# Optimization experiments

Measured on AMD Instinct MI355X. Metric: run time of the kernel, lower is better.

Reference implementation:

```python
import jax, jax.numpy as jnp
import numpy as np

B, C, H, W = 16, 512, 32, 32
CI = C // 2
EPS = 1e-5


def _lin_params(k, din, dout):
    kw, kb = jax.random.split(k)
    w = jax.random.normal(kw, (dout, din), jnp.float32) * (1.0 / np.sqrt(din))
    b = jax.random.normal(kb, (dout,), jnp.float32) * 0.01
    return w, b


def _bn_params(k):
    k1, k2, k3, k4 = jax.random.split(k, 4)
    g = 1.0 + 0.05 * jax.random.normal(k1, (C,), jnp.float32)
    b = 0.05 * jax.random.normal(k2, (C,), jnp.float32)
    m = 0.1 * jax.random.normal(k3, (C,), jnp.float32)
    v = jax.random.uniform(k4, (C,), jnp.float32, 0.5, 1.5)
    return g, b, m, v


def setup_inputs() -> dict:
    key = jax.random.key(0)
    ks = jax.random.split(key, 12)
    inp = {
        'rgb_cm': jax.random.normal(ks[0], (B, C, H, W), jnp.float32),
        'flow_cm': jax.random.normal(ks[1], (B, C, H, W), jnp.float32),
    }
    for i, pfx in enumerate(['1', '2']):
        g, b, m, v = _bn_params(ks[2 + 5 * i])
        inp[f'bn{pfx}_g'], inp[f'bn{pfx}_b'] = g, b
        inp[f'bn{pfx}_m'], inp[f'bn{pfx}_v'] = m, v
        inp[f'th{pfx}_w'], inp[f'th{pfx}_b'] = _lin_params(ks[3 + 5 * i], C, CI)
        inp[f'ph{pfx}_w'], inp[f'ph{pfx}_b'] = _lin_params(ks[4 + 5 * i], C, CI)
        inp[f'g{pfx}_w'], inp[f'g{pfx}_b'] = _lin_params(ks[5 + 5 * i], C, CI)
        inp[f'w{pfx}_w'], inp[f'w{pfx}_b'] = _lin_params(ks[6 + 5 * i], CI, C)
    return inp


def _bn_relu(x, g, b, m, v):
    # x: [B, C, num]; eval-mode BatchNorm1d over channel dim, then ReLU
    scale = (g * jax.lax.rsqrt(v + EPS))[None, :, None]
    shift = (b - m * g * jax.lax.rsqrt(v + EPS))[None, :, None]
    return jax.nn.relu(x * scale + shift)


def _can(A, Bx, bn_g, bn_b, bn_m, bn_v, th_w, th_b, ph_w, ph_b, g_w, g_b, w_w, w_b):
    # A, Bx: [B, C, num]
    A = _bn_relu(A, bn_g, bn_b, bn_m, bn_v).transpose(0, 2, 1)   # [B, num, C]
    Bx = _bn_relu(Bx, bn_g, bn_b, bn_m, bn_v).transpose(0, 2, 1)  # [B, num, C]
    x_theta = A @ th_w.T + th_b      # [B, num, CI]
    x_phi = Bx @ ph_w.T + ph_b       # [B, num, CI]
    attn = jnp.einsum('bnc,bmc->bnm', x_theta, x_phi)  # [B, num, num] (unscaled)
    f_div_C = jax.nn.softmax(attn, axis=-1)
    g_x = A @ g_w.T + g_b            # [B, num, CI]
    y = jnp.einsum('bnm,bmc->bnc', f_div_C, g_x)
    W_y = y @ w_w.T + w_b            # [B, num, C]
    return (A + W_y).transpose(0, 2, 1)  # [B, C, num]


def reference(rgb_cm, flow_cm,
              bn1_g, bn1_b, bn1_m, bn1_v, th1_w, th1_b, ph1_w, ph1_b, g1_w, g1_b, w1_w, w1_b,
              bn2_g, bn2_b, bn2_m, bn2_v, th2_w, th2_b, ph2_w, ph2_b, g2_w, g2_b, w2_w, w2_b):
    b, c, h, w = rgb_cm.shape
    rgb_f = rgb_cm.reshape(b, c, h * w)
    flow_f = flow_cm.reshape(b, c, h * w)
    att_rgb = _can(rgb_f, flow_f, bn1_g, bn1_b, bn1_m, bn1_v,
                   th1_w, th1_b, ph1_w, ph1_b, g1_w, g1_b, w1_w, w1_b)
    att_flow = _can(flow_f, rgb_f, bn2_g, bn2_b, bn2_m, bn2_v,
                    th2_w, th2_b, ph2_w, ph2_b, g2_w, g2_b, w2_w, w2_b)
    return att_rgb.reshape(b, c, h, w), att_flow.reshape(b, c, h, w)
```

## Files before the change

kernel.cpp:

```cpp
#include <hip/hip_runtime.h>


typedef __bf16 bf16x8 __attribute__((ext_vector_type(8)));
typedef float  f32x4  __attribute__((ext_vector_type(4)));
typedef float  f32x16 __attribute__((ext_vector_type(16)));
typedef unsigned u32x4 __attribute__((ext_vector_type(4)));
static_assert(sizeof(bf16x8) == 16, "bf16x8 must be 16B");

constexpr int KTILE = 8704;
constexpr int VTILE = 10240;
constexpr int KINST = 32 * KTILE;
constexpr int VINST = 32 * VTILE;

__device__ __forceinline__ ushort f2bf(float x) {
  unsigned u = __builtin_bit_cast(unsigned, x);
  u = (u + 0x7fffu + ((u >> 16) & 1u)) >> 16;
  return (ushort)u;
}
__device__ __forceinline__ unsigned packbf(float lo, float hi) {
  return (unsigned)f2bf(lo) | ((unsigned)f2bf(hi) << 16);
}
__device__ __forceinline__ void gload_lds16(const ushort* g, ushort* l) {
  __builtin_amdgcn_global_load_lds(
      (const __attribute__((address_space(1))) void*)g,
      (__attribute__((address_space(3))) void*)l, 16, 0, 0);
}

struct WcvtArgs { const float* src[8]; };
__global__ __launch_bounds__(256) void wcvt8_k(WcvtArgs a, ushort* __restrict__ dst) {
  const int which = blockIdx.y;
  const int i = (blockIdx.x * 256 + threadIdx.x) * 4;
  float4 x = *reinterpret_cast<const float4*>(a.src[which] + i);
  ushort4 u = {f2bf(x.x), f2bf(x.y), f2bf(x.z), f2bf(x.w)};
  *reinterpret_cast<ushort4*>(dst + (size_t)which * 131072 + i) = u;
}

__global__ __launch_bounds__(256) void bn2_k(
    const float* __restrict__ rgb, const float* __restrict__ flow,
    const float* __restrict__ g1, const float* __restrict__ b1,
    const float* __restrict__ m1, const float* __restrict__ v1,
    const float* __restrict__ g2, const float* __restrict__ b2,
    const float* __restrict__ m2, const float* __restrict__ v2,
    ushort* __restrict__ Abn1, ushort* __restrict__ Bbn1,
    ushort* __restrict__ Abn2, ushort* __restrict__ Bbn2)
{
  const int z = blockIdx.z;
  const int b = z >> 1, which = z & 1;
  const float* src = which ? flow : rgb;
  ushort* o1 = which ? Bbn1 : Abn1;
  ushort* o2 = which ? Abn2 : Bbn2;
  src += (size_t)b * 512 * 1024;
  o1  += (size_t)b * 1024 * 512;
  o2  += (size_t)b * 1024 * 512;

  __shared__ unsigned tileU[32][36];
  const int n0 = blockIdx.x * 32, c0 = blockIdx.y * 32;

  const int rc = threadIdx.x >> 3, nq = threadIdx.x & 7;
  {
    const int c = c0 + rc;
    const float s1 = g1[c] * rsqrtf(v1[c] + 1e-5f);
    const float h1 = b1[c] - m1[c] * s1;
    const float s2 = g2[c] * rsqrtf(v2[c] + 1e-5f);
    const float h2 = b2[c] - m2[c] * s2;
    float4 x = *reinterpret_cast<const float4*>(src + (size_t)c * 1024 + n0 + nq * 4);
    u32x4 u;
    u[0] = packbf(fmaxf(x.x * s1 + h1, 0.f), fmaxf(x.x * s2 + h2, 0.f));
    u[1] = packbf(fmaxf(x.y * s1 + h1, 0.f), fmaxf(x.y * s2 + h2, 0.f));
    u[2] = packbf(fmaxf(x.z * s1 + h1, 0.f), fmaxf(x.z * s2 + h2, 0.f));
    u[3] = packbf(fmaxf(x.w * s1 + h1, 0.f), fmaxf(x.w * s2 + h2, 0.f));
    *reinterpret_cast<u32x4*>(&tileU[rc][nq * 4]) = u;
  }
  __syncthreads();
  const int r = threadIdx.x >> 3, cq = threadIdx.x & 7;
  ushort4 w1, w2;
  {
    const unsigned u0 = tileU[cq * 4 + 0][r];
    const unsigned u1 = tileU[cq * 4 + 1][r];
    const unsigned u2 = tileU[cq * 4 + 2][r];
    const unsigned u3 = tileU[cq * 4 + 3][r];
    w1 = (ushort4){(ushort)(u0 & 0xffff), (ushort)(u1 & 0xffff),
                   (ushort)(u2 & 0xffff), (ushort)(u3 & 0xffff)};
    w2 = (ushort4){(ushort)(u0 >> 16), (ushort)(u1 >> 16),
                   (ushort)(u2 >> 16), (ushort)(u3 >> 16)};
  }
  const size_t base = (size_t)(n0 + r) * 512 + c0 + cq * 4;
  *reinterpret_cast<ushort4*>(o1 + base) = w1;
  *reinterpret_cast<ushort4*>(o2 + base) = w2;
}

struct ProjDesc { const ushort* W; const ushort* act; const float* bias;
                  ushort* out; int mode; };
struct ProjArgs { ProjDesc d[6]; };

__global__ __launch_bounds__(256, 2) void proj128_k(ProjArgs pa) {
  __shared__ __align__(16) ushort Al[128 * 80];
  __shared__ __align__(16) ushort Bl[128 * 80];

  const int bx = blockIdx.x;
  const int mb = bx >> 3, nb = bx & 7;
  const int by = blockIdx.y;
  const ProjDesc d = pa.d[by >> 4];
  const int inst = by & 15;
  const ushort* A = d.W;
  const ushort* Bact = d.act + (size_t)inst * 524288;

  const int tid = threadIdx.x;
  const int w = tid >> 6, lane = tid & 63;
  const int q = lane >> 4, lm = lane & 15;
  const int m0 = mb * 128, n0 = nb * 128;

  int row[4], c8[4];
  #pragma unroll
  for (int i = 0; i < 4; ++i) { int g = i * 256 + tid; row[i] = g >> 3; c8[i] = g & 7; }

  bf16x8 ast[4], bst[4];
  auto sload = [&](int kk) {
    #pragma unroll
    for (int i = 0; i < 4; ++i) {
      ast[i] = *reinterpret_cast<const bf16x8*>(A + (size_t)(m0 + row[i]) * 512 + kk + c8[i] * 8);
      bst[i] = *reinterpret_cast<const bf16x8*>(Bact + (size_t)(n0 + row[i]) * 512 + kk + c8[i] * 8);
    }
  };
  sload(0);

  f32x4 acc[4][4];
  #pragma unroll
  for (int i = 0; i < 4; ++i)
    #pragma unroll
    for (int j = 0; j < 4; ++j) acc[i][j] = (f32x4){0.f, 0.f, 0.f, 0.f};

  const int wm = (w >> 1) * 64, wn = (w & 1) * 64;

  for (int t = 0; t < 8; ++t) {
    __syncthreads();
    #pragma unroll
    for (int i = 0; i < 4; ++i) {
      *reinterpret_cast<bf16x8*>(Al + row[i] * 80 + c8[i] * 8) = ast[i];
      *reinterpret_cast<bf16x8*>(Bl + row[i] * 80 + c8[i] * 8) = bst[i];
    }
    __syncthreads();
    if (t < 7) sload((t + 1) * 64);
    #pragma unroll
    for (int ks = 0; ks < 2; ++ks) {
      bf16x8 af[4], bfr[4];
      #pragma unroll
      for (int f = 0; f < 4; ++f)
        af[f] = *reinterpret_cast<const bf16x8*>(Al + (wm + f * 16 + lm) * 80 + ks * 32 + q * 8);
      #pragma unroll
      for (int f = 0; f < 4; ++f)
        bfr[f] = *reinterpret_cast<const bf16x8*>(Bl + (wn + f * 16 + lm) * 80 + ks * 32 + q * 8);
      __builtin_amdgcn_s_setprio(1);
      #pragma unroll
      for (int fi = 0; fi < 4; ++fi)
        #pragma unroll
        for (int fj = 0; fj < 4; ++fj)
          acc[fi][fj] = __builtin_amdgcn_mfma_f32_16x16x32_bf16(af[fi], bfr[fj], acc[fi][fj], 0, 0, 0);
      __builtin_amdgcn_s_setprio(0);
    }
  }

  if (d.mode == 0) {
    ushort* out = d.out + (size_t)inst * 262144;
    #pragma unroll
    for (int fi = 0; fi < 4; ++fi)
      #pragma unroll
      for (int fj = 0; fj < 4; ++fj) {
        const int m4 = m0 + wm + fi * 16 + q * 4;
        const int n  = n0 + wn + fj * 16 + lm;
        float4 bi = *reinterpret_cast<const float4*>(d.bias + m4);
        ushort4 u = {f2bf(acc[fi][fj][0] + bi.x), f2bf(acc[fi][fj][1] + bi.y),
                     f2bf(acc[fi][fj][2] + bi.z), f2bf(acc[fi][fj][3] + bi.w)};
        *reinterpret_cast<ushort4*>(out + (size_t)n * 256 + m4) = u;
      }
  } else if (d.mode == 1) {
    ushort* out = d.out + (size_t)inst * KINST;
    #pragma unroll
    for (int fi = 0; fi < 4; ++fi)
      #pragma unroll
      for (int fj = 0; fj < 4; ++fj) {
        const int m4 = m0 + wm + fi * 16 + q * 4;
        const int n  = n0 + wn + fj * 16 + lm;
        float4 bi = *reinterpret_cast<const float4*>(d.bias + m4);
        ushort4 u = {f2bf(acc[fi][fj][0] + bi.x), f2bf(acc[fi][fj][1] + bi.y),
                     f2bf(acc[fi][fj][2] + bi.z), f2bf(acc[fi][fj][3] + bi.w)};
        *reinterpret_cast<ushort4*>(out + (size_t)(n >> 5) * KTILE + (n & 31) * 264 + m4) = u;
      }
  } else {
    ushort* out = d.out + (size_t)inst * VINST;
    #pragma unroll
    for (int fi = 0; fi < 4; ++fi)
      #pragma unroll
      for (int fj = 0; fj < 4; ++fj) {
        const int n = n0 + wn + fj * 16 + lm;
        const size_t base = (size_t)(n >> 5) * VTILE + ((n & 31) >> 3) * 8 + (n & 7);
        #pragma unroll
        for (int j = 0; j < 4; ++j) {
          const int m = m0 + wm + fi * 16 + q * 4 + j;
          out[base + (size_t)m * 40] = f2bf(acc[fi][fj][j] + d.bias[m]);
        }
      }
  }
}

__global__ __launch_bounds__(256, 2) void flash_k(
    const ushort* __restrict__ Qp, const ushort* __restrict__ Kg,
    const ushort* __restrict__ Vg, ushort* __restrict__ Op)
{
  __shared__ __align__(16) ushort KV[2][KTILE + VTILE];
  __shared__ float2 stat2[2][32];

  const int raw = blockIdx.x;
  const int xcd = raw & 7, loc = raw >> 3;
  const int inst = xcd * 4 + (loc >> 4);
  const int qb = loc & 15;

  const int tid = threadIdx.x;
  const int w = tid >> 6, lane = tid & 63;
  const int u = w & 1, p = w >> 1;
  const int h = lane >> 5, lm5 = lane & 31;

  const ushort* Q  = Qp + (size_t)inst * 262144;
  const ushort* Kt = Kg + (size_t)inst * KINST + (size_t)p * 16 * KTILE;
  const ushort* Vt = Vg + (size_t)inst * VINST + (size_t)p * 16 * VTILE;

  ushort* Klds = &KV[p][0];
  ushort* Vlds = &KV[p][KTILE];

  const int nrow0 = qb * 64 + u * 32;

  bf16x8 qf[16];
  #pragma unroll
  for (int cs = 0; cs < 16; ++cs)
    qf[cs] = *reinterpret_cast<const bf16x8*>(
        Q + (size_t)(nrow0 + lm5) * 256 + cs * 16 + h * 8);

  f32x16 acc[8];
  #pragma unroll
  for (int cb = 0; cb < 8; ++cb)
    #pragma unroll
    for (int i = 0; i < 16; ++i) acc[cb][i] = 0.f;

  float run_m = -__builtin_inff();
  float run_l = 0.f;

  auto stageK = [&](int t) {
    const ushort* src = Kt + (size_t)t * KTILE;
    const int base = u ? 9 : 0;
    #pragma unroll
    for (int j = 0; j < 9; ++j)
      if (u == 0 || j < 8)
        gload_lds16(src + (base + j) * 512 + lane * 8, Klds + (base + j) * 512);
  };
  auto stageV = [&](int t) {
    const ushort* src = Vt + (size_t)t * VTILE;
    #pragma unroll
    for (int j = 0; j < 10; ++j)
      gload_lds16(src + (u * 10 + j) * 512 + lane * 8, Vlds + (u * 10 + j) * 512);
  };

  stageK(0);
  stageV(0);
  asm volatile("s_waitcnt vmcnt(0)" ::: "memory");
  __builtin_amdgcn_sched_barrier(0);
  __builtin_amdgcn_s_barrier();

  for (int t = 0; t < 16; ++t) {
    f32x16 S;
    #pragma unroll
    for (int i = 0; i < 16; ++i) S[i] = 0.f;
    __builtin_amdgcn_s_setprio(1);
    #pragma unroll
    for (int cs = 0; cs < 16; ++cs) {
      bf16x8 kf = *reinterpret_cast<const bf16x8*>(
          Klds + lm5 * 264 + (cs * 2 + h) * 8);
      S = __builtin_amdgcn_mfma_f32_32x32x16_bf16(kf, qf[cs], S, 0, 0, 0);
    }
    __builtin_amdgcn_s_setprio(0);

    __builtin_amdgcn_sched_barrier(0);
    asm volatile("s_waitcnt vmcnt(0)" ::: "memory");
    __builtin_amdgcn_sched_barrier(0);
    __builtin_amdgcn_s_barrier();
    __builtin_amdgcn_sched_barrier(0);
    if (t < 15) stageK(t + 1);

    float ml = fmaxf(fmaxf(fmaxf(S[0], S[1]), fmaxf(S[2], S[3])),
                     fmaxf(fmaxf(S[4], S[5]), fmaxf(S[6], S[7])));
    ml = fmaxf(ml, fmaxf(fmaxf(fmaxf(S[8], S[9]), fmaxf(S[10], S[11])),
                         fmaxf(fmaxf(S[12], S[13]), fmaxf(S[14], S[15]))));
    ml = fmaxf(ml, __shfl_xor(ml, 32));
    const float mnew = fmaxf(run_m, ml);
    if (!__all(ml <= run_m + 8.f)) {
      const float sc = __expf(run_m - mnew);
      run_m = mnew;
      run_l *= sc;
      #pragma unroll
      for (int cb = 0; cb < 8; ++cb) acc[cb] *= sc;
    }
    #pragma unroll
    for (int i = 0; i < 16; ++i) S[i] = __expf(S[i] - run_m);
    float ts = ((S[0] + S[1]) + (S[2] + S[3])) + ((S[4] + S[5]) + (S[6] + S[7]));
    ts += ((S[8] + S[9]) + (S[10] + S[11])) + ((S[12] + S[13]) + (S[14] + S[15]));
    ts += __shfl_xor(ts, 32);
    run_l += ts;

    const unsigned pk0 = packbf(S[0], S[1]),   pk1 = packbf(S[2], S[3]);
    const unsigned pk2 = packbf(S[4], S[5]),   pk3 = packbf(S[6], S[7]);
    const unsigned pk4 = packbf(S[8], S[9]),   pk5 = packbf(S[10], S[11]);
    const unsigned pk6 = packbf(S[12], S[13]), pk7 = packbf(S[14], S[15]);
    const unsigned sx0 = __shfl_xor(pk0, 32), sx1 = __shfl_xor(pk1, 32);
    const unsigned sx2 = __shfl_xor(pk2, 32), sx3 = __shfl_xor(pk3, 32);
    const unsigned sx4 = __shfl_xor(pk4, 32), sx5 = __shfl_xor(pk5, 32);
    const unsigned sx6 = __shfl_xor(pk6, 32), sx7 = __shfl_xor(pk7, 32);
    const bool hh = (h != 0);
    u32x4 B0, B1;
    B0[0] = hh ? sx2 : pk0;  B0[1] = hh ? sx3 : pk1;
    B0[2] = hh ? pk2 : sx0;  B0[3] = hh ? pk3 : sx1;
    B1[0] = hh ? sx6 : pk4;  B1[1] = hh ? sx7 : pk5;
    B1[2] = hh ? pk6 : sx4;  B1[3] = hh ? pk7 : sx5;
    const bf16x8 pf0 = __builtin_bit_cast(bf16x8, B0);
    const bf16x8 pf1 = __builtin_bit_cast(bf16x8, B1);

    __builtin_amdgcn_s_setprio(1);
    #pragma unroll
    for (int cb = 0; cb < 8; ++cb) {
      bf16x8 v0 = *reinterpret_cast<const bf16x8*>(
          Vlds + (cb * 32 + lm5) * 40 + h * 8);
      bf16x8 v1 = *reinterpret_cast<const bf16x8*>(
          Vlds + (cb * 32 + lm5) * 40 + (2 + h) * 8);
      acc[cb] = __builtin_amdgcn_mfma_f32_32x32x16_bf16(v0, pf0, acc[cb], 0, 0, 0);
      acc[cb] = __builtin_amdgcn_mfma_f32_32x32x16_bf16(v1, pf1, acc[cb], 0, 0, 0);
    }
    __builtin_amdgcn_s_setprio(0);

    __builtin_amdgcn_sched_barrier(0);
    __builtin_amdgcn_s_barrier();
    __builtin_amdgcn_sched_barrier(0);
    if (t < 15) {
      stageV(t + 1);
      asm volatile("s_waitcnt vmcnt(10)" ::: "memory");
    } else {
      asm volatile("s_waitcnt vmcnt(0)" ::: "memory");
    }
    __builtin_amdgcn_sched_barrier(0);
    __builtin_amdgcn_s_barrier();
    __builtin_amdgcn_sched_barrier(0);
  }

  __syncthreads();
  if (p == 1 && lane < 32) stat2[u][lm5] = make_float2(run_m, run_l);

  float a0 = 1.f, a1 = 0.f, inv = 1.f;
  float4* mb = reinterpret_cast<float4*>(&KV[0][0]);
  #pragma unroll
  for (int half = 0; half < 2; ++half) {
    __syncthreads();
    if (p == 1) {
      #pragma unroll
      for (int cb2 = 0; cb2 < 4; ++cb2) {
        const int cb = half * 4 + cb2;
        #pragma unroll
        for (int r4 = 0; r4 < 4; ++r4) {
          float4 v = {acc[cb][r4 * 4 + 0], acc[cb][r4 * 4 + 1],
                      acc[cb][r4 * 4 + 2], acc[cb][r4 * 4 + 3]};
          mb[u * 1024 + cb2 * 256 + r4 * 64 + lane] = v;
        }
      }
    }
    __syncthreads();
    if (p == 0) {
      if (half == 0) {
        const float2 s1 = stat2[u][lm5];
        const float M = fmaxf(run_m, s1.x);
        a0 = __expf(run_m - M);
        a1 = __expf(s1.x - M);
        inv = 1.f / (a0 * run_l + a1 * s1.y);
      }
      ushort* Ob = Op + (size_t)inst * 262144 + (size_t)(nrow0 + lm5) * 256;
      #pragma unroll
      for (int cb2 = 0; cb2 < 4; ++cb2) {
        const int cb = half * 4 + cb2;
        #pragma unroll
        for (int r4 = 0; r4 < 4; ++r4) {
          float4 o = mb[u * 1024 + cb2 * 256 + r4 * 64 + lane];
          ushort4 s;
          s.x = f2bf((a0 * acc[cb][r4 * 4 + 0] + a1 * o.x) * inv);
          s.y = f2bf((a0 * acc[cb][r4 * 4 + 1] + a1 * o.y) * inv);
          s.z = f2bf((a0 * acc[cb][r4 * 4 + 2] + a1 * o.z) * inv);
          s.w = f2bf((a0 * acc[cb][r4 * 4 + 3] + a1 * o.w) * inv);
          *reinterpret_cast<ushort4*>(Ob + cb * 32 + r4 * 8 + h * 4) = s;
        }
      }
    }
  }
}

struct WgemmArgs {
  const ushort* yb[2]; const ushort* wW[2]; const float* wb[2];
  const float* src[2]; const float* g[2]; const float* bb[2];
  const float* mm[2]; const float* vv[2];
};

__global__ __launch_bounds__(256, 2) void wgemm_epi_k(WgemmArgs a, float* __restrict__ outp) {
  __shared__ __align__(16) ushort Al[128 * 80];
  __shared__ __align__(16) ushort Bl[128 * 80];

  const int bx = blockIdx.x;
  const int mb = bx >> 2, nb = bx & 3;
  const int by = blockIdx.y;
  const int mod = by >> 4, b = by & 15;

  const ushort* A  = a.yb[mod] + (size_t)b * 262144;
  const ushort* Bw = a.wW[mod];
  const float* wb  = a.wb[mod];
  const float* src = a.src[mod] + (size_t)b * 512 * 1024;
  const float* g   = a.g[mod];
  const float* bbp = a.bb[mod];
  const float* mm  = a.mm[mod];
  const float* vv  = a.vv[mod];
  float* out = outp + (size_t)mod * 16 * 512 * 1024 + (size_t)b * 512 * 1024;

  const int tid = threadIdx.x;
  const int w = tid >> 6, lane = tid & 63;
  const int q = lane >> 4, lm = lane & 15;
  const int m0 = mb * 128, n0 = nb * 128;

  int row[4], c8[4];
  #pragma unroll
  for (int i = 0; i < 4; ++i) { int gg = i * 256 + tid; row[i] = gg >> 3; c8[i] = gg & 7; }

  bf16x8 ast[4], bst[4];
  auto sload = [&](int kk) {
    #pragma unroll
    for (int i = 0; i < 4; ++i) {
      ast[i] = *reinterpret_cast<const bf16x8*>(A  + (size_t)(m0 + row[i]) * 256 + kk + c8[i] * 8);
      bst[i] = *reinterpret_cast<const bf16x8*>(Bw + (size_t)(n0 + row[i]) * 256 + kk + c8[i] * 8);
    }
  };
  sload(0);

  f32x4 acc[4][4];
  #pragma unroll
  for (int i = 0; i < 4; ++i)
    #pragma unroll
    for (int j = 0; j < 4; ++j) acc[i][j] = (f32x4){0.f, 0.f, 0.f, 0.f};

  const int wm = (w >> 1) * 64, wn = (w & 1) * 64;

  for (int t = 0; t < 4; ++t) {
    __syncthreads();
    #pragma unroll
    for (int i = 0; i < 4; ++i) {
      *reinterpret_cast<bf16x8*>(Al + row[i] * 80 + c8[i] * 8) = ast[i];
      *reinterpret_cast<bf16x8*>(Bl + row[i] * 80 + c8[i] * 8) = bst[i];
    }
    __syncthreads();
    if (t < 3) sload((t + 1) * 64);
    #pragma unroll
    for (int ks = 0; ks < 2; ++ks) {
      bf16x8 af[4], bfr[4];
      #pragma unroll
      for (int f = 0; f < 4; ++f)
        af[f] = *reinterpret_cast<const bf16x8*>(Al + (wm + f * 16 + lm) * 80 + ks * 32 + q * 8);
      #pragma unroll
      for (int f = 0; f < 4; ++f)
        bfr[f] = *reinterpret_cast<const bf16x8*>(Bl + (wn + f * 16 + lm) * 80 + ks * 32 + q * 8);
      __builtin_amdgcn_s_setprio(1);
      #pragma unroll
      for (int fi = 0; fi < 4; ++fi)
        #pragma unroll
        for (int fj = 0; fj < 4; ++fj)
          acc[fi][fj] = __builtin_amdgcn_mfma_f32_16x16x32_bf16(af[fi], bfr[fj], acc[fi][fj], 0, 0, 0);
      __builtin_amdgcn_s_setprio(0);
    }
  }

  #pragma unroll
  for (int fj = 0; fj < 4; ++fj) {
    const int c = n0 + wn + fj * 16 + lm;
    const float sc = g[c] * rsqrtf(vv[c] + 1e-5f);
    const float sh = bbp[c] - mm[c] * sc;
    const float bv = wb[c];
    #pragma unroll
    for (int fi = 0; fi < 4; ++fi) {
      const int n4 = m0 + wm + fi * 16 + q * 4;
      const size_t base = (size_t)c * 1024 + n4;
      float4 x = *reinterpret_cast<const float4*>(src + base);
      float4 v;
      v.x = acc[fi][fj][0] + bv + fmaxf(x.x * sc + sh, 0.f);
      v.y = acc[fi][fj][1] + bv + fmaxf(x.y * sc + sh, 0.f);
      v.z = acc[fi][fj][2] + bv + fmaxf(x.z * sc + sh, 0.f);
      v.w = acc[fi][fj][3] + bv + fmaxf(x.w * sc + sh, 0.f);
      *reinterpret_cast<float4*>(out + base) = v;
    }
  }
}

constexpr size_t MB = 1ull << 20;
constexpr size_t OFF_WBF = 0;
constexpr size_t OFF_BN  = 2 * MB;
constexpr size_t OFF_TH  = 66 * MB;
constexpr size_t OFF_KG  = 82 * MB;
constexpr size_t OFF_VG  = 100 * MB;
constexpr size_t OFF_YB  = 120 * MB;

extern "C" void kernel_launch(void* const* d_in, const int* in_sizes, int n_in,
                              void* d_out, int out_size, void* d_ws, size_t ws_size,
                              hipStream_t stream) {
  const float* rgb  = (const float*)d_in[0];
  const float* flow = (const float*)d_in[1];
  auto in = [&](int mod, int j) { return (const float*)d_in[2 + mod * 12 + j]; };

  char* ws = (char*)d_ws;
  ushort* wbf  = (ushort*)(ws + OFF_WBF);
  ushort* Abn1 = (ushort*)(ws + OFF_BN);
  ushort* Bbn1 = (ushort*)(ws + OFF_BN + 16 * MB);
  ushort* Abn2 = (ushort*)(ws + OFF_BN + 32 * MB);
  ushort* Bbn2 = (ushort*)(ws + OFF_BN + 48 * MB);
  ushort* th   = (ushort*)(ws + OFF_TH);
  ushort* Kgx  = (ushort*)(ws + OFF_KG);
  ushort* Vgx  = (ushort*)(ws + OFF_VG);
  ushort* yb   = (ushort*)(ws + OFF_YB);
  float*  out  = (float*)d_out;

  const size_t MODSTR = (size_t)16 * 262144;

  WcvtArgs wa;
  for (int mod = 0; mod < 2; ++mod) {
    wa.src[mod * 4 + 0] = in(mod, 4);
    wa.src[mod * 4 + 1] = in(mod, 6);
    wa.src[mod * 4 + 2] = in(mod, 8);
    wa.src[mod * 4 + 3] = in(mod, 10);
  }
  wcvt8_k<<<dim3(128, 8), 256, 0, stream>>>(wa, wbf);

  bn2_k<<<dim3(32, 16, 32), 256, 0, stream>>>(
      rgb, flow,
      in(0, 0), in(0, 1), in(0, 2), in(0, 3),
      in(1, 0), in(1, 1), in(1, 2), in(1, 3),
      Abn1, Bbn1, Abn2, Bbn2);

  ProjArgs pa;
  for (int mod = 0; mod < 2; ++mod) {
    const ushort* wb4 = wbf + (size_t)mod * 4 * 131072;
    ushort* Abn = mod ? Abn2 : Abn1;
    ushort* Bbn = mod ? Bbn2 : Bbn1;
    pa.d[mod * 3 + 0] = {wb4,              Abn, in(mod, 5), th + mod * MODSTR,               0};
    pa.d[mod * 3 + 1] = {wb4 + 131072,     Bbn, in(mod, 7), Kgx + (size_t)mod * 16 * KINST, 1};
    pa.d[mod * 3 + 2] = {wb4 + 2 * 131072, Abn, in(mod, 9), Vgx + (size_t)mod * 16 * VINST, 2};
  }
  proj128_k<<<dim3(16, 96), 256, 0, stream>>>(pa);

  flash_k<<<dim3(512), 256, 0, stream>>>(th, Kgx, Vgx, yb);

  WgemmArgs ga;
  for (int mod = 0; mod < 2; ++mod) {
    ga.yb[mod]  = yb + mod * MODSTR;
    ga.wW[mod]  = wbf + (size_t)(mod * 4 + 3) * 131072;
    ga.wb[mod]  = in(mod, 11);
    ga.src[mod] = mod ? flow : rgb;
    ga.g[mod]   = in(mod, 0);
    ga.bb[mod]  = in(mod, 1);
    ga.mm[mod]  = in(mod, 2);
    ga.vv[mod]  = in(mod, 3);
  }
  wgemm_epi_k<<<dim3(32, 32), 256, 0, stream>>>(ga, out);
}
```

Measured before the change: 168.1 us.

## Stage GEMM tiles via direct global-to-LDS loads and raise occupancy

Both the projection GEMM and the output-projection GEMM now fill shared memory with global_load_lds DMA-style loads instead of loading into registers and then writing to LDS. Waves 0-1 fill the A tile and waves 2-3 the B tile, with each lane's offsets precomputed to match the padded 80-element row stride. Padding slots get a dummy load from column 0. Freeing the staging registers allows launch bounds of 4 blocks per CU. The cost is that the old register prefetch overlap is lost: each k-step now waits for its load to complete between two barriers, so global latency is exposed unless occupancy hides it.

```diff
diff --git a/kernel.cpp b/kernel.cpp
--- a/kernel.cpp
+++ b/kernel.cpp
@@ -93,7 +93,7 @@
                   ushort* out; int mode; };
 struct ProjArgs { ProjDesc d[6]; };
 
-__global__ __launch_bounds__(256, 2) void proj128_k(ProjArgs pa) {
+__global__ __launch_bounds__(256, 4) void proj128_k(ProjArgs pa) {
   __shared__ __align__(16) ushort Al[128 * 80];
   __shared__ __align__(16) ushort Bl[128 * 80];
 
@@ -110,19 +110,24 @@
   const int q = lane >> 4, lm = lane & 15;
   const int m0 = mb * 128, n0 = nb * 128;
 
-  int row[4], c8[4];
-  #pragma unroll
-  for (int i = 0; i < 4; ++i) { int g = i * 256 + tid; row[i] = g >> 3; c8[i] = g & 7; }
-
-  bf16x8 ast[4], bst[4];
-  auto sload = [&](int kk) {
-    #pragma unroll
-    for (int i = 0; i < 4; ++i) {
-      ast[i] = *reinterpret_cast<const bf16x8*>(A + (size_t)(m0 + row[i]) * 512 + kk + c8[i] * 8);
-      bst[i] = *reinterpret_cast<const bf16x8*>(Bact + (size_t)(n0 + row[i]) * 512 + kk + c8[i] * 8);
-    }
+  const bool isA = (w < 2);
+  const ushort* gbase = isA ? (A + (size_t)m0 * 512) : (Bact + (size_t)n0 * 512);
+  ushort* lbase = (isA ? Al : Bl) + ((w & 1) * 10) * 512;
+  int roff[10];
+  #pragma unroll
+  for (int i = 0; i < 10; ++i) {
+    const int j = (w & 1) * 10 + i;
+    const int off = j * 512 + lane * 8;
+    const int row = off / 80;
+    int col = off - row * 80;
+    if (col >= 64) col = 0;
+    roff[i] = row * 512 + col;
+  }
+  auto stage = [&](int kk) {
+    #pragma unroll
+    for (int i = 0; i < 10; ++i)
+      gload_lds16(gbase + roff[i] + kk, lbase + i * 512);
   };
-  sload(0);
 
   f32x4 acc[4][4];
   #pragma unroll
@@ -132,15 +137,11 @@
 
   const int wm = (w >> 1) * 64, wn = (w & 1) * 64;
 
+  stage(0);
+  asm volatile("s_waitcnt vmcnt(0)" ::: "memory");
+  __syncthreads();
+
   for (int t = 0; t < 8; ++t) {
-    __syncthreads();
-    #pragma unroll
-    for (int i = 0; i < 4; ++i) {
-      *reinterpret_cast<bf16x8*>(Al + row[i] * 80 + c8[i] * 8) = ast[i];
-      *reinterpret_cast<bf16x8*>(Bl + row[i] * 80 + c8[i] * 8) = bst[i];
-    }
-    __syncthreads();
-    if (t < 7) sload((t + 1) * 64);
     #pragma unroll
     for (int ks = 0; ks < 2; ++ks) {
       bf16x8 af[4], bfr[4];
@@ -157,6 +158,12 @@
         for (int fj = 0; fj < 4; ++fj)
           acc[fi][fj] = __builtin_amdgcn_mfma_f32_16x16x32_bf16(af[fi], bfr[fj], acc[fi][fj], 0, 0, 0);
       __builtin_amdgcn_s_setprio(0);
+    }
+    if (t < 7) {
+      __syncthreads();
+      stage((t + 1) * 64);
+      asm volatile("s_waitcnt vmcnt(0)" ::: "memory");
+      __syncthreads();
     }
   }
 
@@ -402,7 +409,7 @@
   const float* mm[2]; const float* vv[2];
 };
 
-__global__ __launch_bounds__(256, 2) void wgemm_epi_k(WgemmArgs a, float* __restrict__ outp) {
+__global__ __launch_bounds__(256, 4) void wgemm_epi_k(WgemmArgs a, float* __restrict__ outp) {
   __shared__ __align__(16) ushort Al[128 * 80];
   __shared__ __align__(16) ushort Bl[128 * 80];
 
@@ -426,19 +433,24 @@
   const int q = lane >> 4, lm = lane & 15;
   const int m0 = mb * 128, n0 = nb * 128;
 
-  int row[4], c8[4];
-  #pragma unroll
-  for (int i = 0; i < 4; ++i) { int gg = i * 256 + tid; row[i] = gg >> 3; c8[i] = gg & 7; }
-
-  bf16x8 ast[4], bst[4];
-  auto sload = [&](int kk) {
-    #pragma unroll
-    for (int i = 0; i < 4; ++i) {
-      ast[i] = *reinterpret_cast<const bf16x8*>(A  + (size_t)(m0 + row[i]) * 256 + kk + c8[i] * 8);
-      bst[i] = *reinterpret_cast<const bf16x8*>(Bw + (size_t)(n0 + row[i]) * 256 + kk + c8[i] * 8);
-    }
+  const bool isA = (w < 2);
+  const ushort* gbase = isA ? (A + (size_t)m0 * 256) : (Bw + (size_t)n0 * 256);
+  ushort* lbase = (isA ? Al : Bl) + ((w & 1) * 10) * 512;
+  int roff[10];
+  #pragma unroll
+  for (int i = 0; i < 10; ++i) {
+    const int j = (w & 1) * 10 + i;
+    const int off = j * 512 + lane * 8;
+    const int row = off / 80;
+    int col = off - row * 80;
+    if (col >= 64) col = 0;
+    roff[i] = row * 256 + col;
+  }
+  auto stage = [&](int kk) {
+    #pragma unroll
+    for (int i = 0; i < 10; ++i)
+      gload_lds16(gbase + roff[i] + kk, lbase + i * 512);
   };
-  sload(0);
 
   f32x4 acc[4][4];
   #pragma unroll
@@ -448,15 +460,11 @@
 
   const int wm = (w >> 1) * 64, wn = (w & 1) * 64;
 
+  stage(0);
+  asm volatile("s_waitcnt vmcnt(0)" ::: "memory");
+  __syncthreads();
+
   for (int t = 0; t < 4; ++t) {
-    __syncthreads();
-    #pragma unroll
-    for (int i = 0; i < 4; ++i) {
-      *reinterpret_cast<bf16x8*>(Al + row[i] * 80 + c8[i] * 8) = ast[i];
-      *reinterpret_cast<bf16x8*>(Bl + row[i] * 80 + c8[i] * 8) = bst[i];
-    }
-    __syncthreads();
-    if (t < 3) sload((t + 1) * 64);
     #pragma unroll
     for (int ks = 0; ks < 2; ++ks) {
       bf16x8 af[4], bfr[4];
@@ -473,6 +481,12 @@
         for (int fj = 0; fj < 4; ++fj)
           acc[fi][fj] = __builtin_amdgcn_mfma_f32_16x16x32_bf16(af[fi], bfr[fj], acc[fi][fj], 0, 0, 0);
       __builtin_amdgcn_s_setprio(0);
+    }
+    if (t < 3) {
+      __syncthreads();
+      stage((t + 1) * 64);
+      asm volatile("s_waitcnt vmcnt(0)" ::: "memory");
+      __syncthreads();
     }
   }
 
```

Measured after the change: 175.3 us. 1.04x slower.
